# Optimization experiments

Measured on AMD Instinct MI355X. Metric: run time of the kernel, lower is better.

The kernel has to match this reference:

```python
import jax, jax.numpy as jnp
import numpy as np

EPS = 1.0  # Shapelet eps
STRIDE = 1


def _shapelet(x, w, pcm):
    """x: (b,c,t), w: (n,c,l), pcm: (c,m). Returns ((b, n*c) probs, (b, n*c) dists)."""
    n, c, l = w.shape
    t = x.shape[-1]
    m = (t - l) // STRIDE + 1
    # unfold: gather overlapping windows -> (b, c, m, l)
    idx = jnp.arange(m)[:, None] * STRIDE + jnp.arange(l)[None, :]
    win = x[:, :, idx]                                   # (b, c, m, l)
    xw = jnp.transpose(win, (0, 2, 1, 3))[:, :, None]    # (b, m, 1, c, l)
    d = jnp.mean(jnp.abs(xw - w), axis=-1)               # (b, m, n, c)
    d = d * pcm.T[None, :, None, :]                      # penalty (1, m, 1, c)
    p = jnp.exp(-jnp.square(EPS * d))                    # (b, m, n, c)
    hard = jax.nn.one_hot(jnp.argmax(p, axis=1), m, axis=1, dtype=p.dtype)  # (b,m,n,c)
    soft = jax.nn.softmax(p, axis=1)
    onehot_max = hard + soft - jax.lax.stop_gradient(soft)  # straight-through
    max_p = jnp.sum(onehot_max * p, axis=1)              # (b, n, c)
    d_min = jnp.min(d, axis=1)                           # (b, n, c)
    b = x.shape[0]
    return max_p.reshape(b, -1), d_min.reshape(b, -1)


def _diversity(w):
    """w: (n,c,l) -> scalar. torch PairwiseDistance(p=2, eps=1e-6) adds eps to diff."""
    sh = jnp.transpose(w, (1, 0, 2))                     # (c, n, l)
    diff = sh[:, None, :, :] - sh[:, :, None, :] + 1e-6
    dist = jnp.sqrt(jnp.sum(jnp.square(diff), axis=-1))  # (c, n, n)
    nsh = sh.shape[1]
    mask = 1.0 - jnp.eye(nsh, dtype=w.dtype)
    return jnp.mean(jnp.exp(-dist) * mask[None])


def setup_inputs() -> dict:
    key = jax.random.key(0)
    ks = jax.random.split(key, 6)
    b, c, t, ncls = 32, 8, 512, 10
    sls = [52, 103, 154, 256]
    ms = [t - l + 1 for l in sls]
    inp = {"x": jax.random.normal(ks[0], (b, c, t), dtype=jnp.float32)}
    for i, (l, m) in enumerate(zip(sls, ms)):
        inp[f"w{i}"] = jax.random.normal(ks[1 + i], (5, c, l), dtype=jnp.float32)
        inp[f"pcm{i}"] = jnp.ones((c, m), dtype=jnp.float32)
    inp["W_out"] = jax.random.normal(ks[5], (ncls, 160), dtype=jnp.float32) * 0.05
    return inp


def reference(x, w0, w1, w2, w3, pcm0, pcm1, pcm2, pcm3, W_out):
    # instance norm over time (torch std is unbiased, ddof=1)
    mu = jnp.mean(x, axis=-1, keepdims=True)
    sd = jnp.std(x, axis=-1, keepdims=True, ddof=1)
    xn = (x - mu) / (sd + 1e-8)

    ws = (w0, w1, w2, w3)
    pcms = (pcm0, pcm1, pcm2, pcm3)
    probs, dists = [], []
    for w, pcm in zip(ws, pcms):
        p, d = _shapelet(xn, w, pcm)
        probs.append(p)
        dists.append(d)
    shapelet_probs = jnp.concatenate(probs, axis=-1)   # (b, 160)
    shapelet_dists = jnp.concatenate(dists, axis=-1)   # (b, 160)

    # dropout is identity in eval mode
    out = shapelet_probs @ W_out.T                     # (b, num_classes)

    loss_reg = jnp.mean(jnp.abs(W_out))
    loss_div = sum(_diversity(w) for w in ws)
    loss = (0.1 * loss_reg + 0.1 * loss_div).reshape(1)
    return out, shapelet_dists, shapelet_probs, loss
```

## Files before the change

kernel.cpp:

```cpp
#include <hip/hip_runtime.h>
#include <math.h>

#define B 32
#define C 8
#define T 512
#define NSH 5
#define NCLS 10
#define NFEAT 160

#define OUT_OFF    0
#define DIST_OFF   (B * NCLS)
#define PROB_OFF   (DIST_OFF + B * NFEAT)
#define LOSS_OFF   (PROB_OFF + B * NFEAT)


__global__ __launch_bounds__(256) void shapelet_kernel(
    const float* __restrict__ x,
    const float* __restrict__ w0, const float* __restrict__ w1,
    const float* __restrict__ w2, const float* __restrict__ w3,
    const float* __restrict__ p0, const float* __restrict__ p1,
    const float* __restrict__ p2, const float* __restrict__ p3,
    const float* __restrict__ Wout,
    float* __restrict__ out, float* __restrict__ wsf)
{
    const int tid = threadIdx.x;

    if (blockIdx.y == 4) {
        const int bc = blockIdx.x;
        __shared__ float part[4];
        const int wv   = tid >> 6;
        const int lane = tid & 63;
        if (bc < 160) {
            const int task = bc * 4 + wv;
            const int g  = task / 160;
            const int r  = task - g * 160;
            const int c  = r / 20;
            const int pr = r - c * 20;
            const int i  = pr >> 2;
            const int j0 = pr & 3;
            const int j  = j0 + (j0 >= i ? 1 : 0);
            const float* wptrs[4] = { w0, w1, w2, w3 };
            const int    Ls[4]    = { 52, 103, 154, 256 };
            const int L = Ls[g];
            const float* wi = wptrs[g] + (i * C + c) * L;
            const float* wj = wptrs[g] + (j * C + c) * L;
            float ss = 0.0f;
            for (int t2 = lane; t2 < L; t2 += 64) {
                const float df = wj[t2] - wi[t2] + 1e-6f;
                ss += df * df;
            }
            #pragma unroll
            for (int off = 32; off; off >>= 1) ss += __shfl_down(ss, off);
            if (lane == 0) part[wv] = expf(-sqrtf(ss));
            __syncthreads();
            if (tid == 0) wsf[bc] = part[0] + part[1] + part[2] + part[3];
        } else if (bc < 168) {
            float rg = 0.0f;
            if (tid < 200) rg = fabsf(Wout[(bc - 160) * 200 + tid]);
            #pragma unroll
            for (int off = 32; off; off >>= 1) rg += __shfl_down(rg, off);
            if ((tid & 63) == 0) part[wv] = rg;
            __syncthreads();
            if (tid == 0) wsf[bc] = part[0] + part[1] + part[2] + part[3];
        }
        return;
    }

    const int bc = blockIdx.x;
    const int g  = blockIdx.y;
    const int b  = bc >> 3;
    const int c  = bc & 7;

    const float* wptr; const float* pptr; int L, M, goff;
    switch (g) {
        case 0:  wptr = w0; pptr = p0; L = 52;  M = 461; goff = 0;   break;
        case 1:  wptr = w1; pptr = p1; L = 103; M = 410; goff = 40;  break;
        case 2:  wptr = w2; pptr = p2; L = 154; M = 359; goff = 80;  break;
        default: wptr = w3; pptr = p3; L = 256; M = 257; goff = 120; break;
    }
    const int Lp = (L + 3) & ~3;

    __shared__ __align__(16) float xs[T + 4];
    __shared__ __align__(16) float ws[NSH * 256];
    __shared__ __align__(16) float pm[464];
    __shared__ float wred[8];

    const float v0 = x[bc * T + tid];
    const float v1 = x[bc * T + tid + 256];
    float s = v0 + v1;
    #pragma unroll
    for (int off = 32; off; off >>= 1) s += __shfl_down(s, off);
    if ((tid & 63) == 0) wred[tid >> 6] = s;
    __syncthreads();
    const float mu = (wred[0] + wred[1] + wred[2] + wred[3]) * (1.0f / T);
    __syncthreads();
    const float d0 = v0 - mu, d1 = v1 - mu;
    float sq = d0 * d0 + d1 * d1;
    #pragma unroll
    for (int off = 32; off; off >>= 1) sq += __shfl_down(sq, off);
    if ((tid & 63) == 0) wred[tid >> 6] = sq;
    __syncthreads();
    const float var = (wred[0] + wred[1] + wred[2] + wred[3]) * (1.0f / (T - 1));
    const float inv = 1.0f / (sqrtf(var) + 1e-8f);
    xs[tid]       = d0 * inv;
    xs[tid + 256] = d1 * inv;
    if (tid < 4) xs[T + tid] = 0.0f;

    for (int i = tid; i < NSH * Lp; i += 256) {
        const int n = i / Lp, j = i - n * Lp;
        ws[i] = (j < L) ? wptr[(n * C + c) * L + j] : 0.0f;
    }
    for (int i = tid; i < 464; i += 256) pm[i] = (i < M) ? pptr[c * M + i] : 0.0f;
    __syncthreads();

    const float invL = 1.0f / (float)L;
    const int sbase = tid * 4;
    const bool active = (sbase < M);
    float* dists = out + DIST_OFF + b * NFEAT;
    float* probs = out + PROB_OFF + b * NFEAT;

    float pm0 = 0, pm1 = 0, pm2 = 0, pm3 = 0;
    if (active) {
        const float4 pv = *(const float4*)(pm + sbase);
        pm0 = pv.x; pm1 = pv.y; pm2 = pv.z; pm3 = pv.w;
    }

    for (int n = 0; n < NSH; ++n) {
        float a0 = 0, a1 = 0, a2 = 0, a3 = 0;
        if (active) {
            const float* wn = ws + n * Lp;
            float4 cur = *(const float4*)(xs + sbase);
            int j = 0;
            for (; j + 4 <= L; j += 4) {
                const float4 nxt = *(const float4*)(xs + sbase + j + 4);
                const float4 wv  = *(const float4*)(wn + j);
                a0 += fabsf(cur.x - wv.x); a1 += fabsf(cur.y - wv.x);
                a2 += fabsf(cur.z - wv.x); a3 += fabsf(cur.w - wv.x);
                a0 += fabsf(cur.y - wv.y); a1 += fabsf(cur.z - wv.y);
                a2 += fabsf(cur.w - wv.y); a3 += fabsf(nxt.x - wv.y);
                a0 += fabsf(cur.z - wv.z); a1 += fabsf(cur.w - wv.z);
                a2 += fabsf(nxt.x - wv.z); a3 += fabsf(nxt.y - wv.z);
                a0 += fabsf(cur.w - wv.w); a1 += fabsf(nxt.x - wv.w);
                a2 += fabsf(nxt.y - wv.w); a3 += fabsf(nxt.z - wv.w);
                cur = nxt;
            }
            for (; j < L; ++j) {
                const float wj = wn[j];
                a0 += fabsf(xs[sbase + j]     - wj);
                a1 += fabsf(xs[sbase + j + 1] - wj);
                a2 += fabsf(xs[sbase + j + 2] - wj);
                a3 += fabsf(xs[sbase + j + 3] - wj);
            }
        }
        float mind = INFINITY, mind2 = INFINITY;
        if (active) {
            const float dd0 = a0 * invL * pm0;
            mind = dd0; mind2 = dd0 * dd0;
            if (sbase + 1 < M) { const float dd = a1 * invL * pm1; mind = fminf(mind, dd); mind2 = fminf(mind2, dd * dd); }
            if (sbase + 2 < M) { const float dd = a2 * invL * pm2; mind = fminf(mind, dd); mind2 = fminf(mind2, dd * dd); }
            if (sbase + 3 < M) { const float dd = a3 * invL * pm3; mind = fminf(mind, dd); mind2 = fminf(mind2, dd * dd); }
        }
        #pragma unroll
        for (int off = 32; off; off >>= 1) {
            mind  = fminf(mind,  __shfl_down(mind,  off));
            mind2 = fminf(mind2, __shfl_down(mind2, off));
        }
        __syncthreads();
        if ((tid & 63) == 0) { wred[tid >> 6] = mind; wred[4 + (tid >> 6)] = mind2; }
        __syncthreads();
        if (tid == 0) {
            const float md  = fminf(fminf(wred[0], wred[1]), fminf(wred[2], wred[3]));
            const float md2 = fminf(fminf(wred[4], wred[5]), fminf(wred[6], wred[7]));
            const int col = goff + n * C + c;
            dists[col] = md;
            probs[col] = expf(-md2);
        }
    }
}

__global__ __launch_bounds__(64) void head_kernel(
    const float* __restrict__ Wout,
    const float* __restrict__ wsf,
    float* __restrict__ out)
{
    const int blk  = blockIdx.x;
    const int lane = threadIdx.x;
    if (blk < B * NCLS) {
        const int b = blk / NCLS, k = blk - b * NCLS;
        const float* pr = out + PROB_OFF + b * NFEAT;
        const float* wr = Wout + k * NFEAT;
        float acc = 0.0f;
        #pragma unroll
        for (int r = 0; r < 3; ++r) {
            const int f = lane + r * 64;
            if (f < NFEAT) acc += pr[f] * wr[f];
        }
        #pragma unroll
        for (int off = 32; off; off >>= 1) acc += __shfl_down(acc, off);
        if (lane == 0) out[OUT_OFF + blk] = acc;
    } else {
        float dv = 0.0f, rg = 0.0f;
        #pragma unroll
        for (int r = 0; r < 3; ++r) {
            const int i = lane + r * 64;
            if (i < 160) dv += wsf[i];
            else if (i < 168) rg += wsf[i];
        }
        #pragma unroll
        for (int off = 32; off; off >>= 1) {
            dv += __shfl_down(dv, off);
            rg += __shfl_down(rg, off);
        }
        if (lane == 0)
            out[LOSS_OFF] = 0.1f * (rg * (1.0f / 1600.0f)) + 0.1f * (dv * (1.0f / 200.0f));
    }
}

extern "C" void kernel_launch(void* const* d_in, const int* in_sizes, int n_in,
                              void* d_out, int out_size, void* d_ws, size_t ws_size,
                              hipStream_t stream) {
    const float* x    = (const float*)d_in[0];
    const float* w0   = (const float*)d_in[1];
    const float* pcm0 = (const float*)d_in[2];
    const float* w1   = (const float*)d_in[3];
    const float* pcm1 = (const float*)d_in[4];
    const float* w2   = (const float*)d_in[5];
    const float* pcm2 = (const float*)d_in[6];
    const float* w3   = (const float*)d_in[7];
    const float* pcm3 = (const float*)d_in[8];
    const float* Wout = (const float*)d_in[9];
    float* out = (float*)d_out;
    float* wsf = (float*)d_ws;

    shapelet_kernel<<<dim3(256, 5), 256, 0, stream>>>(
        x, w0, w1, w2, w3, pcm0, pcm1, pcm2, pcm3, Wout, out, wsf);
    head_kernel<<<B * NCLS + 1, 64, 0, stream>>>(Wout, wsf, out);
}
```

Measured before the change: 123.7 us.

## Map each (b,c,group,shapelet) task to one wavefront without shared memory

Restructures the shapelet kernel so each 64-lane wavefront owns one (batch, channel, group, shapelet) task. Each lane computes 8 window positions in registers, reading x and weights directly from global memory and recomputing the instance norm per wave. This removes the shared-memory staging, block-level syncthreads and the serial loop over shapelets, and specialises L and M at compile time via templates. In exchange every wave redundantly normalises its row, and weight values are read from global or cache as scalar loads rather than from LDS.

```diff
diff --git a/kernel.cpp b/kernel.cpp
--- a/kernel.cpp
+++ b/kernel.cpp
@@ -13,6 +13,96 @@
 #define PROB_OFF   (DIST_OFF + B * NFEAT)
 #define LOSS_OFF   (PROB_OFF + B * NFEAT)
 
+
+template<int L, int M, int GOFF>
+__device__ __forceinline__ void shapelet_task(
+    const float* __restrict__ x,
+    const float* __restrict__ wrow,
+    const float* __restrict__ pmrow,
+    float* __restrict__ out, int bc, int n)
+{
+    const int lane = threadIdx.x & 63;
+    const int b = bc >> 3, c = bc & 7;
+    const float* xrow = x + bc * T;
+
+    const float4 u0 = *(const float4*)(xrow + lane * 4);
+    const float4 u1 = *(const float4*)(xrow + 256 + lane * 4);
+    float s = u0.x + u0.y + u0.z + u0.w + u1.x + u1.y + u1.z + u1.w;
+    #pragma unroll
+    for (int off = 32; off; off >>= 1) s += __shfl_down(s, off);
+    const float mu = __shfl(s, 0) * (1.0f / T);
+    float sq = (u0.x-mu)*(u0.x-mu) + (u0.y-mu)*(u0.y-mu) + (u0.z-mu)*(u0.z-mu) + (u0.w-mu)*(u0.w-mu)
+             + (u1.x-mu)*(u1.x-mu) + (u1.y-mu)*(u1.y-mu) + (u1.z-mu)*(u1.z-mu) + (u1.w-mu)*(u1.w-mu);
+    #pragma unroll
+    for (int off = 32; off; off >>= 1) sq += __shfl_down(sq, off);
+    const float var = __shfl(sq, 0) * (1.0f / (T - 1));
+    const float ns = 1.0f / (sqrtf(var) + 1e-8f);
+    const float nb = -mu * ns;
+
+    const int sbase = lane * 8;
+    const int sb = (sbase < M) ? sbase : 0;
+
+    float4 a  = *(const float4*)(xrow + sb);
+    float4 bb = *(const float4*)(xrow + sb + 4);
+    float4 cc = *(const float4*)(xrow + sb + 8);
+    a.x = fmaf(a.x, ns, nb);  a.y = fmaf(a.y, ns, nb);  a.z = fmaf(a.z, ns, nb);  a.w = fmaf(a.w, ns, nb);
+    bb.x = fmaf(bb.x, ns, nb); bb.y = fmaf(bb.y, ns, nb); bb.z = fmaf(bb.z, ns, nb); bb.w = fmaf(bb.w, ns, nb);
+    cc.x = fmaf(cc.x, ns, nb); cc.y = fmaf(cc.y, ns, nb); cc.z = fmaf(cc.z, ns, nb); cc.w = fmaf(cc.w, ns, nb);
+
+    float acc[8] = {0,0,0,0,0,0,0,0};
+    constexpr int LC = L & ~3;
+
+    #pragma unroll 4
+    for (int j = 0; j + 4 <= L; j += 4) {
+        const float wa = wrow[j], wb = wrow[j+1], wc = wrow[j+2], wd = wrow[j+3];
+        acc[0]+=fabsf(a.x-wa); acc[1]+=fabsf(a.y-wa); acc[2]+=fabsf(a.z-wa); acc[3]+=fabsf(a.w-wa);
+        acc[4]+=fabsf(bb.x-wa); acc[5]+=fabsf(bb.y-wa); acc[6]+=fabsf(bb.z-wa); acc[7]+=fabsf(bb.w-wa);
+        acc[0]+=fabsf(a.y-wb); acc[1]+=fabsf(a.z-wb); acc[2]+=fabsf(a.w-wb); acc[3]+=fabsf(bb.x-wb);
+        acc[4]+=fabsf(bb.y-wb); acc[5]+=fabsf(bb.z-wb); acc[6]+=fabsf(bb.w-wb); acc[7]+=fabsf(cc.x-wb);
+        acc[0]+=fabsf(a.z-wc); acc[1]+=fabsf(a.w-wc); acc[2]+=fabsf(bb.x-wc); acc[3]+=fabsf(bb.y-wc);
+        acc[4]+=fabsf(bb.z-wc); acc[5]+=fabsf(bb.w-wc); acc[6]+=fabsf(cc.x-wc); acc[7]+=fabsf(cc.y-wc);
+        acc[0]+=fabsf(a.w-wd); acc[1]+=fabsf(bb.x-wd); acc[2]+=fabsf(bb.y-wd); acc[3]+=fabsf(bb.z-wd);
+        acc[4]+=fabsf(bb.w-wd); acc[5]+=fabsf(cc.x-wd); acc[6]+=fabsf(cc.y-wd); acc[7]+=fabsf(cc.z-wd);
+        a = bb; bb = cc;
+        int nidx = sb + j + 12;
+        nidx = (nidx > T - 4) ? (T - 4) : nidx;
+        cc = *(const float4*)(xrow + nidx);
+        cc.x = fmaf(cc.x, ns, nb); cc.y = fmaf(cc.y, ns, nb);
+        cc.z = fmaf(cc.z, ns, nb); cc.w = fmaf(cc.w, ns, nb);
+    }
+
+    if constexpr ((L & 3) != 0) {
+        const float rr[12] = {a.x,a.y,a.z,a.w, bb.x,bb.y,bb.z,bb.w, cc.x,cc.y,cc.z,cc.w};
+        #pragma unroll
+        for (int jt = 0; jt < (L & 3); ++jt) {
+            const float wj = wrow[LC + jt];
+            #pragma unroll
+            for (int k = 0; k < 8; ++k) acc[k] += fabsf(rr[jt + k] - wj);
+        }
+    }
+
+    constexpr float invL = 1.0f / (float)L;
+    float mind = INFINITY, mind2 = INFINITY;
+    #pragma unroll
+    for (int k = 0; k < 8; ++k) {
+        const int m = sbase + k;
+        if (m < M) {
+            const float d = acc[k] * invL * pmrow[m];
+            mind  = fminf(mind, d);
+            mind2 = fminf(mind2, d * d);
+        }
+    }
+    #pragma unroll
+    for (int off = 32; off; off >>= 1) {
+        mind  = fminf(mind,  __shfl_down(mind,  off));
+        mind2 = fminf(mind2, __shfl_down(mind2, off));
+    }
+    if (lane == 0) {
+        const int col = GOFF + n * C + c;
+        out[DIST_OFF + b * NFEAT + col] = mind;
+        out[PROB_OFF + b * NFEAT + col] = expf(-mind2);
+    }
+}
 
 __global__ __launch_bounds__(256) void shapelet_kernel(
     const float* __restrict__ x,
@@ -23,158 +113,55 @@
     const float* __restrict__ Wout,
     float* __restrict__ out, float* __restrict__ wsf)
 {
-    const int tid = threadIdx.x;
-
-    if (blockIdx.y == 4) {
-        const int bc = blockIdx.x;
-        __shared__ float part[4];
-        const int wv   = tid >> 6;
-        const int lane = tid & 63;
-        if (bc < 160) {
-            const int task = bc * 4 + wv;
-            const int g  = task / 160;
-            const int r  = task - g * 160;
-            const int c  = r / 20;
-            const int pr = r - c * 20;
-            const int i  = pr >> 2;
-            const int j0 = pr & 3;
-            const int j  = j0 + (j0 >= i ? 1 : 0);
-            const float* wptrs[4] = { w0, w1, w2, w3 };
-            const int    Ls[4]    = { 52, 103, 154, 256 };
-            const int L = Ls[g];
-            const float* wi = wptrs[g] + (i * C + c) * L;
-            const float* wj = wptrs[g] + (j * C + c) * L;
-            float ss = 0.0f;
-            for (int t2 = lane; t2 < L; t2 += 64) {
-                const float df = wj[t2] - wi[t2] + 1e-6f;
-                ss += df * df;
-            }
-            #pragma unroll
-            for (int off = 32; off; off >>= 1) ss += __shfl_down(ss, off);
-            if (lane == 0) part[wv] = expf(-sqrtf(ss));
-            __syncthreads();
-            if (tid == 0) wsf[bc] = part[0] + part[1] + part[2] + part[3];
-        } else if (bc < 168) {
-            float rg = 0.0f;
-            if (tid < 200) rg = fabsf(Wout[(bc - 160) * 200 + tid]);
-            #pragma unroll
-            for (int off = 32; off; off >>= 1) rg += __shfl_down(rg, off);
-            if ((tid & 63) == 0) part[wv] = rg;
-            __syncthreads();
-            if (tid == 0) wsf[bc] = part[0] + part[1] + part[2] + part[3];
-        }
-        return;
-    }
-
-    const int bc = blockIdx.x;
-    const int g  = blockIdx.y;
-    const int b  = bc >> 3;
-    const int c  = bc & 7;
-
-    const float* wptr; const float* pptr; int L, M, goff;
-    switch (g) {
-        case 0:  wptr = w0; pptr = p0; L = 52;  M = 461; goff = 0;   break;
-        case 1:  wptr = w1; pptr = p1; L = 103; M = 410; goff = 40;  break;
-        case 2:  wptr = w2; pptr = p2; L = 154; M = 359; goff = 80;  break;
-        default: wptr = w3; pptr = p3; L = 256; M = 257; goff = 120; break;
-    }
-    const int Lp = (L + 3) & ~3;
-
-    __shared__ __align__(16) float xs[T + 4];
-    __shared__ __align__(16) float ws[NSH * 256];
-    __shared__ __align__(16) float pm[464];
-    __shared__ float wred[8];
-
-    const float v0 = x[bc * T + tid];
-    const float v1 = x[bc * T + tid + 256];
-    float s = v0 + v1;
-    #pragma unroll
-    for (int off = 32; off; off >>= 1) s += __shfl_down(s, off);
-    if ((tid & 63) == 0) wred[tid >> 6] = s;
-    __syncthreads();
-    const float mu = (wred[0] + wred[1] + wred[2] + wred[3]) * (1.0f / T);
-    __syncthreads();
-    const float d0 = v0 - mu, d1 = v1 - mu;
-    float sq = d0 * d0 + d1 * d1;
-    #pragma unroll
-    for (int off = 32; off; off >>= 1) sq += __shfl_down(sq, off);
-    if ((tid & 63) == 0) wred[tid >> 6] = sq;
-    __syncthreads();
-    const float var = (wred[0] + wred[1] + wred[2] + wred[3]) * (1.0f / (T - 1));
-    const float inv = 1.0f / (sqrtf(var) + 1e-8f);
-    xs[tid]       = d0 * inv;
-    xs[tid + 256] = d1 * inv;
-    if (tid < 4) xs[T + tid] = 0.0f;
-
-    for (int i = tid; i < NSH * Lp; i += 256) {
-        const int n = i / Lp, j = i - n * Lp;
-        ws[i] = (j < L) ? wptr[(n * C + c) * L + j] : 0.0f;
-    }
-    for (int i = tid; i < 464; i += 256) pm[i] = (i < M) ? pptr[c * M + i] : 0.0f;
-    __syncthreads();
-
-    const float invL = 1.0f / (float)L;
-    const int sbase = tid * 4;
-    const bool active = (sbase < M);
-    float* dists = out + DIST_OFF + b * NFEAT;
-    float* probs = out + PROB_OFF + b * NFEAT;
-
-    float pm0 = 0, pm1 = 0, pm2 = 0, pm3 = 0;
-    if (active) {
-        const float4 pv = *(const float4*)(pm + sbase);
-        pm0 = pv.x; pm1 = pv.y; pm2 = pv.z; pm3 = pv.w;
-    }
-
-    for (int n = 0; n < NSH; ++n) {
-        float a0 = 0, a1 = 0, a2 = 0, a3 = 0;
-        if (active) {
-            const float* wn = ws + n * Lp;
-            float4 cur = *(const float4*)(xs + sbase);
-            int j = 0;
-            for (; j + 4 <= L; j += 4) {
-                const float4 nxt = *(const float4*)(xs + sbase + j + 4);
-                const float4 wv  = *(const float4*)(wn + j);
-                a0 += fabsf(cur.x - wv.x); a1 += fabsf(cur.y - wv.x);
-                a2 += fabsf(cur.z - wv.x); a3 += fabsf(cur.w - wv.x);
-                a0 += fabsf(cur.y - wv.y); a1 += fabsf(cur.z - wv.y);
-                a2 += fabsf(cur.w - wv.y); a3 += fabsf(nxt.x - wv.y);
-                a0 += fabsf(cur.z - wv.z); a1 += fabsf(cur.w - wv.z);
-                a2 += fabsf(nxt.x - wv.z); a3 += fabsf(nxt.y - wv.z);
-                a0 += fabsf(cur.w - wv.w); a1 += fabsf(nxt.x - wv.w);
-                a2 += fabsf(nxt.y - wv.w); a3 += fabsf(nxt.z - wv.w);
-                cur = nxt;
-            }
-            for (; j < L; ++j) {
-                const float wj = wn[j];
-                a0 += fabsf(xs[sbase + j]     - wj);
-                a1 += fabsf(xs[sbase + j + 1] - wj);
-                a2 += fabsf(xs[sbase + j + 2] - wj);
-                a3 += fabsf(xs[sbase + j + 3] - wj);
-            }
-        }
-        float mind = INFINITY, mind2 = INFINITY;
-        if (active) {
-            const float dd0 = a0 * invL * pm0;
-            mind = dd0; mind2 = dd0 * dd0;
-            if (sbase + 1 < M) { const float dd = a1 * invL * pm1; mind = fminf(mind, dd); mind2 = fminf(mind2, dd * dd); }
-            if (sbase + 2 < M) { const float dd = a2 * invL * pm2; mind = fminf(mind, dd); mind2 = fminf(mind2, dd * dd); }
-            if (sbase + 3 < M) { const float dd = a3 * invL * pm3; mind = fminf(mind, dd); mind2 = fminf(mind2, dd * dd); }
-        }
-        #pragma unroll
-        for (int off = 32; off; off >>= 1) {
-            mind  = fminf(mind,  __shfl_down(mind,  off));
-            mind2 = fminf(mind2, __shfl_down(mind2, off));
-        }
-        __syncthreads();
-        if ((tid & 63) == 0) { wred[tid >> 6] = mind; wred[4 + (tid >> 6)] = mind2; }
-        __syncthreads();
-        if (tid == 0) {
-            const float md  = fminf(fminf(wred[0], wred[1]), fminf(wred[2], wred[3]));
-            const float md2 = fminf(fminf(wred[4], wred[5]), fminf(wred[6], wred[7]));
-            const int col = goff + n * C + c;
-            dists[col] = md;
-            probs[col] = expf(-md2);
-        }
+    const int blk = blockIdx.x;
+    const int wv  = __builtin_amdgcn_readfirstlane(threadIdx.x >> 6);
+
+    if (blk < 1280) {
+        const int bc = blk / 5;
+        const int gn = (blk - bc * 5) * 4 + wv;
+        const int g  = gn / 5;
+        const int n  = gn - g * 5;
+        const int c  = bc & 7;
+        switch (g) {
+            case 0: shapelet_task< 52, 461,   0>(x, w0 + (n*C+c)*52,  p0 + c*461, out, bc, n); break;
+            case 1: shapelet_task<103, 410,  40>(x, w1 + (n*C+c)*103, p1 + c*410, out, bc, n); break;
+            case 2: shapelet_task<154, 359,  80>(x, w2 + (n*C+c)*154, p2 + c*359, out, bc, n); break;
+            default:shapelet_task<256, 257, 120>(x, w3 + (n*C+c)*256, p3 + c*257, out, bc, n); break;
+        }
+    } else if (blk < 1440) {
+        const int task = (blk - 1280) * 4 + wv;
+        const int lane = threadIdx.x & 63;
+        const int g  = task / 160;
+        const int r  = task - g * 160;
+        const int c  = r / 20;
+        const int pr = r - c * 20;
+        const int i  = pr >> 2;
+        const int j0 = pr & 3;
+        const int j  = j0 + (j0 >= i ? 1 : 0);
+        const float* wptrs[4] = { w0, w1, w2, w3 };
+        const int    Ls[4]    = { 52, 103, 154, 256 };
+        const int L = Ls[g];
+        const float* wi = wptrs[g] + (i * C + c) * L;
+        const float* wj = wptrs[g] + (j * C + c) * L;
+        float ss = 0.0f;
+        for (int t2 = lane; t2 < L; t2 += 64) {
+            const float df = wj[t2] - wi[t2] + 1e-6f;
+            ss += df * df;
+        }
+        #pragma unroll
+        for (int off = 32; off; off >>= 1) ss += __shfl_down(ss, off);
+        if (lane == 0) wsf[task] = expf(-sqrtf(ss));
+    } else {
+        const int lane = threadIdx.x & 63;
+        float rg = 0.0f;
+        #pragma unroll
+        for (int k2 = 0; k2 < 7; ++k2) {
+            const int e = lane + k2 * 64;
+            if (e < 400) rg += fabsf(Wout[wv * 400 + e]);
+        }
+        #pragma unroll
+        for (int off = 32; off; off >>= 1) rg += __shfl_down(rg, off);
+        if (lane == 0) wsf[640 + wv] = rg;
     }
 }
 
@@ -201,11 +188,11 @@
     } else {
         float dv = 0.0f, rg = 0.0f;
         #pragma unroll
-        for (int r = 0; r < 3; ++r) {
+        for (int r = 0; r < 10; ++r) {
             const int i = lane + r * 64;
-            if (i < 160) dv += wsf[i];
-            else if (i < 168) rg += wsf[i];
-        }
+            if (i < 640) dv += wsf[i];
+        }
+        if (lane < 4) rg = wsf[640 + lane];
         #pragma unroll
         for (int off = 32; off; off >>= 1) {
             dv += __shfl_down(dv, off);
@@ -232,7 +219,7 @@
     float* out = (float*)d_out;
     float* wsf = (float*)d_ws;
 
-    shapelet_kernel<<<dim3(256, 5), 256, 0, stream>>>(
+    shapelet_kernel<<<1441, 256, 0, stream>>>(
         x, w0, w1, w2, w3, pcm0, pcm1, pcm2, pcm3, Wout, out, wsf);
     head_kernel<<<B * NCLS + 1, 64, 0, stream>>>(Wout, wsf, out);
 }
```

Measured after the change: 111.4 us. 10.0% less time.
